# Performance work log

Measured on AMD Instinct MI355X. Metric: run time of the kernel, lower is better.

Reference implementation:

```python
import jax, jax.numpy as jnp
import numpy as np

B, T, D, H = 2, 2048, 1024, 16
DK = D // H


def setup_inputs() -> dict:
    key = jax.random.key(0)
    ks = jax.random.split(key, 9)
    s = 1.0 / np.sqrt(D)
    x = jax.random.normal(ks[0], (B, T, D), dtype=jnp.float32)
    # causal mask (1 = attend, 0 = masked), broadcast over batch and heads
    mask = jnp.tril(jnp.ones((T, T), dtype=jnp.int32))[None, None, :, :]
    Wq = jax.random.uniform(ks[1], (D, D), jnp.float32, -s, s)
    bq = jax.random.uniform(ks[2], (D,), jnp.float32, -s, s)
    Wk = jax.random.uniform(ks[3], (D, D), jnp.float32, -s, s)
    bk = jax.random.uniform(ks[4], (D,), jnp.float32, -s, s)
    Wv = jax.random.uniform(ks[5], (D, D), jnp.float32, -s, s)
    bv = jax.random.uniform(ks[6], (D,), jnp.float32, -s, s)
    Wo = jax.random.uniform(ks[7], (D, D), jnp.float32, -s, s)
    bo = jax.random.uniform(ks[8], (D,), jnp.float32, -s, s)
    return {"x": x, "mask": mask, "Wq": Wq, "bq": bq, "Wk": Wk, "bk": bk,
            "Wv": Wv, "bv": bv, "Wo": Wo, "bo": bo}


def reference(x, mask, Wq, bq, Wk, bk, Wv, bv, Wo, bo):
    # nn.Linear: y = x @ W.T + b
    q = (x @ Wq.T + bq).reshape(B, T, H, DK).transpose(0, 2, 1, 3)  # [B,H,T,DK]
    k = (x @ Wk.T + bk).reshape(B, T, H, DK).transpose(0, 2, 1, 3)
    v = (x @ Wv.T + bv).reshape(B, T, H, DK).transpose(0, 2, 1, 3)
    scores = jnp.einsum('bhqd,bhkd->bhqk', q, k) / np.sqrt(DK).astype(np.float32)
    scores = jnp.where(mask == 0, -jnp.inf, scores)
    attn = jax.nn.softmax(scores, axis=-1)
    out = jnp.einsum('bhqk,bhkd->bhqd', attn, v)  # [B,H,T,DK]
    out = out.transpose(0, 2, 1, 3).reshape(B, T, D)
    return out @ Wo.T + bo
```

## Files before the change

kernel.cpp:

```cpp
#include <hip/hip_runtime.h>

typedef unsigned short u16;
typedef unsigned int u32;
typedef unsigned long long u64;
typedef __attribute__((ext_vector_type(8))) short short8;
typedef __attribute__((ext_vector_type(4))) float f32x4;

#define B_ 2
#define T_ 2048
#define H_ 16
#define DK_ 64
#define QSCALE 0.18033688011112042f

__device__ __forceinline__ u16 f2bf(float f){
  unsigned u = __float_as_uint(f);
  return (u16)((u + 0x7fffu + ((u >> 16) & 1u)) >> 16);
}

__device__ __forceinline__ u32 cvtpk(float lo, float hi){
  u32 r;
  asm("v_cvt_pk_bf16_f32 %0, %1, %2" : "=v"(r) : "v"(lo), "v"(hi));
  return r;
}

#define EXP2(x) __expf(0.6931471805599453f * (x))

__device__ __forceinline__ short8 pack8(const f32x4 a, const f32x4 b){
  union { u32 u[4]; short8 s; } t;
  t.u[0] = cvtpk(a[0], a[1]); t.u[1] = cvtpk(a[2], a[3]);
  t.u[2] = cvtpk(b[0], b[1]); t.u[3] = cvtpk(b[2], b[3]);
  return t.s;
}

#if defined(__has_builtin)
#if __has_builtin(__builtin_amdgcn_global_load_lds)
#define HAS_GLLDS 1
#endif
#endif

#ifdef HAS_GLLDS
__device__ __forceinline__ void gl_lds16(const u16* g, u16* l){
  __builtin_amdgcn_global_load_lds(
      (__attribute__((address_space(1))) void*)(void*)g,
      (__attribute__((address_space(3))) void*)(void*)l, 16, 0, 0);
}
__device__ __forceinline__ void wait_vm4(){ asm volatile("s_waitcnt vmcnt(4)" ::: "memory"); }
__device__ __forceinline__ void wait_vm0(){ asm volatile("s_waitcnt vmcnt(0)" ::: "memory"); }
__device__ __forceinline__ void pipe_bar(){
  asm volatile("" ::: "memory");
  __builtin_amdgcn_s_barrier();
  asm volatile("" ::: "memory");
}
#else
__device__ __forceinline__ void wait_vm4(){}
__device__ __forceinline__ void wait_vm0(){}
__device__ __forceinline__ void pipe_bar(){ __syncthreads(); }
#endif

__global__ __launch_bounds__(256) void conv_all(
    const float* __restrict__ x, const float* __restrict__ wq, const float* __restrict__ wk,
    const float* __restrict__ wv, const float* __restrict__ wo,
    u16* __restrict__ xb, u16* __restrict__ wqb, u16* __restrict__ wkb,
    u16* __restrict__ wvb, u16* __restrict__ wob)
{
  int gid = blockIdx.x * 256 + threadIdx.x;
  const float* src; u16* dst; int off;
  if (gid < 1048576){ src = x; dst = xb; off = gid; }
  else {
    int t = gid - 1048576; int s = t >> 18; off = t & 262143;
    src = (s==0)?wq:((s==1)?wk:((s==2)?wv:wo));
    dst = (s==0)?wqb:((s==1)?wkb:((s==2)?wvb:wob));
  }
  float4 v = ((const float4*)src)[off];
  u64 r = (u64)f2bf(v.x) | ((u64)f2bf(v.y)<<16) | ((u64)f2bf(v.z)<<32) | ((u64)f2bf(v.w)<<48);
  ((u64*)dst)[off] = r;
}

template<int QKV>
__global__ __launch_bounds__(256, 3) void gemm_k5(
    const u16* __restrict__ A,
    const u16* __restrict__ W0, const u16* __restrict__ W1, const u16* __restrict__ W2,
    const float* __restrict__ b0, const float* __restrict__ b1, const float* __restrict__ b2,
    void* __restrict__ o0, void* __restrict__ o1, void* __restrict__ o2)
{
  __shared__ u16 As[3 * 4096];
  __shared__ u16 Bs[3 * 4096];
  const int tid = threadIdx.x;
  const int sel = QKV ? (blockIdx.x >> 3) : 0;
  const int n0 = (blockIdx.x & 7) * 128;
  const int m0 = blockIdx.y * 128;
  const u16* Bw = (sel==0)?W0:((sel==1)?W1:W2);
  const float* bias = (sel==0)?b0:((sel==1)?b1:b2);
  const int w = tid>>6, l = tid&63;
  const int lr = l&15, lg = l>>4;
  const int wm = (w&1)*64, wn = (w>>1)*64;
  const int scol = ((l & 3) ^ ((l >> 3) & 3)) * 8;
  const u16* Ab = A  + (size_t)m0*1024 + (size_t)(l>>2)*1024 + scol;
  const u16* Bb = Bw + (size_t)n0*1024 + (size_t)(l>>2)*1024 + scol;
  const int rsw = (lr >> 1) & 3;
  f32x4 acc[4][4] = {};

  auto STAGE = [&](int t, int pb){
#pragma unroll
    for (int i = 0; i < 2; ++i){
      int c = w*2 + i;
#ifdef HAS_GLLDS
      gl_lds16(Ab + (size_t)(16*c)*1024 + t*32, &As[pb*4096 + c*512]);
      gl_lds16(Bb + (size_t)(16*c)*1024 + t*32, &Bs[pb*4096 + c*512]);
#else
      *(uint4*)&As[pb*4096 + c*512 + l*8] = *(const uint4*)(Ab + (size_t)(16*c)*1024 + t*32);
      *(uint4*)&Bs[pb*4096 + c*512 + l*8] = *(const uint4*)(Bb + (size_t)(16*c)*1024 + t*32);
#endif
    }
  };

  STAGE(0, 0); STAGE(1, 1);
  wait_vm4();
  pipe_bar();
  for (int it = 0; it < 32; ++it){
    const int pb = it % 3;
    if (it < 30) STAGE(it + 2, (it + 2) % 3);
    short8 af[4], bf[4];
#pragma unroll
    for (int mi=0;mi<4;++mi) af[mi] = *(const short8*)&As[pb*4096 + (wm+16*mi+lr)*32 + 8*(lg ^ rsw)];
#pragma unroll
    for (int ni=0;ni<4;++ni) bf[ni] = *(const short8*)&Bs[pb*4096 + (wn+16*ni+lr)*32 + 8*(lg ^ rsw)];
#pragma unroll
    for (int mi=0;mi<4;++mi)
#pragma unroll
      for (int ni=0;ni<4;++ni)
        acc[mi][ni] = __builtin_amdgcn_mfma_f32_16x16x32_bf16(af[mi], bf[ni], acc[mi][ni], 0,0,0);
    if (it < 31){
      if (it < 30) wait_vm4();
      else         wait_vm0();
      pipe_bar();
    }
  }

  float bv[4];
#pragma unroll
  for (int ni=0;ni<4;++ni) bv[ni] = bias[n0+wn+16*ni+lr];
  void* C = QKV ? ((sel==0)?o0:((sel==1)?o1:o2)) : o0;
#pragma unroll
  for (int mi=0;mi<4;++mi)
#pragma unroll
    for (int r=0;r<4;++r){
      const int trow = m0 + wm + 16*mi + 4*lg + r;
#pragma unroll
      for (int ni=0;ni<4;++ni){
        float v = acc[mi][ni][r] + bv[ni];
        int n = n0 + wn + 16*ni + lr;
        if (!QKV){
          ((float*)C)[(size_t)trow*1024 + n] = v;
        } else if (sel == 0){
          ((u16*)C)[(size_t)trow*1024 + n] = f2bf(v * QSCALE);
        } else if (sel == 1){
          int nsw = (n & ~63) | ((n & 63) ^ ((trow & 7) << 3));
          ((u16*)C)[(size_t)trow*1024 + nsw] = f2bf(v);
        } else {
          ((u16*)C)[(size_t)trow*1024 + n] = f2bf(v);
        }
      }
    }
}

__global__ __launch_bounds__(256) void transpose_v128(const u16* __restrict__ V,
                                                      u16* __restrict__ VT){
  __shared__ u16 L[128 * 72];
  const int tid = threadIdx.x;
  const int tc = blockIdx.x, h = blockIdx.y, b = blockIdx.z;
#pragma unroll
  for (int p = 0; p < 4; ++p){
    int row = (tid >> 3) + 32 * p, g = tid & 7;
    *(uint4*)&L[row * 72 + g * 8] =
        *(const uint4*)(V + ((size_t)(b * T_ + tc * 128 + row) * H_ + h) * DK_ + g * 8);
  }
  __syncthreads();
#pragma unroll
  for (int p = 0; p < 4; ++p){
    int d = tid >> 2, g8 = (tid & 3) + 4 * p;
    union { uint4 u; u16 s[8]; } tv;
#pragma unroll
    for (int i = 0; i < 8; ++i){
      int pp = 8 * g8 + i;
      int tl = 32 * (pp >> 5) + 16 * ((pp >> 2) & 1) + 4 * ((pp >> 3) & 3) + (pp & 3);
      tv.s[i] = L[tl * 72 + d];
    }
    *(uint4*)(VT + ((size_t)(b * H_ + h) * DK_ + d) * T_ + tc * 128 + ((8 * g8) ^ ((d & 7) << 3))) = tv.u;
  }
}

__global__ __launch_bounds__(256, 2) void attn_v7(
    const u16* __restrict__ Q, const u16* __restrict__ K,
    const u16* __restrict__ VT, u16* __restrict__ O)
{
  __shared__ u16 Ks[2][128 * 64];
  __shared__ u16 VTs[2][64 * 128];
  const int tid = threadIdx.x;
  const int w = tid >> 6, l = tid & 63;
  const int lr = l & 15, lg = l >> 4;
  const int h = blockIdx.y, b = blockIdx.z;
  const int qtb = (b == 0) ? blockIdx.x : (15 - blockIdx.x);
  const int q0 = qtb * 128;
  const int wrow0 = q0 + 32 * w;
  const size_t kbase = ((size_t)(b * T_) * H_ + h) * DK_;
  const size_t vbase = (size_t)(b * H_ + h) * DK_ * (size_t)T_;

  auto STAGE = [&](int kt, int pb){
#pragma unroll
    for (int p = 0; p < 4; ++p){
      int kr0 = 32 * w + 8 * p;
#ifdef HAS_GLLDS
      gl_lds16(K + kbase + (size_t)(kt * 128 + kr0 + (l >> 3)) * 1024 + (l & 7) * 8,
               &Ks[pb][kr0 * 64]);
#else
      *(uint4*)&Ks[pb][(kr0 + (l >> 3)) * 64 + (l & 7) * 8] =
          *(const uint4*)(K + kbase + (size_t)(kt * 128 + kr0 + (l >> 3)) * 1024 + (l & 7) * 8);
#endif
    }
#pragma unroll
    for (int p = 0; p < 4; ++p){
      int dr0 = 16 * w + 4 * p;
#ifdef HAS_GLLDS
      gl_lds16(VT + vbase + (size_t)(dr0 + (l >> 4)) * T_ + kt * 128 + (l & 15) * 8,
               &VTs[pb][dr0 * 128]);
#else
      *(uint4*)&VTs[pb][(dr0 + (l >> 4)) * 128 + (l & 15) * 8] =
          *(const uint4*)(VT + vbase + (size_t)(dr0 + (l >> 4)) * T_ + kt * 128 + (l & 15) * 8);
#endif
    }
  };

  short8 qf[2][2];
#pragma unroll
  for (int mi = 0; mi < 2; ++mi)
#pragma unroll
    for (int s = 0; s < 2; ++s)
      qf[mi][s] = *(const short8*)(Q + kbase + (size_t)(wrow0 + 16 * mi + lr) * 1024 + s * 32 + 8 * lg);

  f32x4 acc[2][4] = {};
  float lsum[2] = {0.f, 0.f};
  const int ktend = qtb;

  STAGE(0, 0);
  __syncthreads();
  for (int kt = 0; kt <= ktend; ++kt){
    const int pb = kt & 1;
    if (kt < ktend) STAGE(kt + 1, pb ^ 1);
    const bool diag = (kt == ktend);
    short8 pf[2][4];
#pragma unroll
    for (int jh = 0; jh < 2; ++jh){
      short8 kf[4][2];
#pragma unroll
      for (int j = 0; j < 4; ++j)
#pragma unroll
        for (int s = 0; s < 2; ++s)
          kf[j][s] = *(const short8*)&Ks[pb][((4 * jh + j) * 16 + lr) * 64 + (((4 * s + lg) ^ (lr & 7)) << 3)];
#pragma unroll
      for (int mi = 0; mi < 2; ++mi){
        f32x4 pr[4];
        float lacc = 0.f;
        const int lim = 32 * w + 16 * mi + lr;
#pragma unroll
        for (int j = 0; j < 4; ++j){
          const int j0 = 4 * jh + j;
          f32x4 z = {};
          z = __builtin_amdgcn_mfma_f32_16x16x32_bf16(kf[j][0], qf[mi][0], z, 0, 0, 0);
          z = __builtin_amdgcn_mfma_f32_16x16x32_bf16(kf[j][1], qf[mi][1], z, 0, 0, 0);
#pragma unroll
          for (int r = 0; r < 4; ++r){
            float e = EXP2(z[r]);
            if (diag && (16 * j0 + 4 * lg + r > lim)) e = 0.f;
            pr[j][r] = e;
            lacc += e;
          }
        }
        lsum[mi] += lacc;
        pf[mi][2 * jh]     = pack8(pr[0], pr[1]);
        pf[mi][2 * jh + 1] = pack8(pr[2], pr[3]);
      }
    }
#pragma unroll
    for (int ks = 0; ks < 4; ++ks)
#pragma unroll
      for (int d0 = 0; d0 < 4; ++d0){
        short8 vf = *(const short8*)&VTs[pb][(d0 * 16 + lr) * 128 + (((4 * ks + lg) ^ (lr & 7)) << 3)];
        acc[0][d0] = __builtin_amdgcn_mfma_f32_16x16x32_bf16(pf[0][ks], vf, acc[0][d0], 0, 0, 0);
        acc[1][d0] = __builtin_amdgcn_mfma_f32_16x16x32_bf16(pf[1][ks], vf, acc[1][d0], 0, 0, 0);
      }
    __syncthreads();
  }

#pragma unroll
  for (int mi = 0; mi < 2; ++mi){
    float v = lsum[mi];
    v += __shfl_xor(v, 16);
    v += __shfl_xor(v, 32);
    float inv = 1.0f / v;
    float invr[4];
#pragma unroll
    for (int r = 0; r < 4; ++r) invr[r] = __shfl(inv, 4 * lg + r);
#pragma unroll
    for (int d0 = 0; d0 < 4; ++d0)
#pragma unroll
      for (int r = 0; r < 4; ++r){
        float ov = acc[mi][d0][r] * invr[r];
        O[kbase + (size_t)(wrow0 + 16 * mi + 4 * lg + r) * 1024 + d0 * 16 + lr] = f2bf(ov);
      }
  }
}

extern "C" void kernel_launch(void* const* d_in, const int* in_sizes, int n_in,
                              void* d_out, int out_size, void* d_ws, size_t ws_size,
                              hipStream_t stream)
{
  const float* x  = (const float*)d_in[0];
  const float* Wq = (const float*)d_in[2];
  const float* bq = (const float*)d_in[3];
  const float* Wk = (const float*)d_in[4];
  const float* bk = (const float*)d_in[5];
  const float* Wv = (const float*)d_in[6];
  const float* bv = (const float*)d_in[7];
  const float* Wo = (const float*)d_in[8];
  const float* bo = (const float*)d_in[9];

  char* ws = (char*)d_ws;
  u16* xb  = (u16*)(ws + 0);
  u16* wqb = (u16*)(ws + 8388608);
  u16* wkb = (u16*)(ws + 10485760);
  u16* wvb = (u16*)(ws + 12582912);
  u16* wob = (u16*)(ws + 14680064);
  u16* qb  = (u16*)(ws + 16777216);
  u16* kb  = (u16*)(ws + 25165824);
  u16* vb  = (u16*)(ws + 33554432);
  u16* vtb = xb;
  u16* ab  = vb;

  conv_all<<<8192, 256, 0, stream>>>(x, Wq, Wk, Wv, Wo, xb, wqb, wkb, wvb, wob);

  gemm_k5<1><<<dim3(24, 32), 256, 0, stream>>>(
      xb, wqb, wkb, wvb, bq, bk, bv, (void*)qb, (void*)kb, (void*)vb);

  transpose_v128<<<dim3(T_/128, H_, B_), 256, 0, stream>>>(vb, vtb);

  attn_v7<<<dim3(T_/128, H_, B_), 256, 0, stream>>>(qb, kb, vtb, ab);

  gemm_k5<0><<<dim3(8, 32), 256, 0, stream>>>(
      ab, wob, wob, wob, bo, bo, bo, d_out, d_out, d_out);
}
```

Before: 115.5 us.

## Use 256x256-tile 8-wave QKV GEMM with K=64 double buffering

Replaces the 128x128-tile QKV projection GEMM with a 256x256-tile, 512-thread kernel. It uses K-step 64, XOR-swizzled LDS and a double buffer whose next-tile loads are interleaved with MFMA quarters under raised wave priority. The larger tile raises operand reuse and halves the K-loop count. The trade-off is a grid of only 192 blocks on a many-CU device, plus higher LDS and register pressure. The output-projection GEMM is split into its own specialised non-template kernel.

```diff
diff --git a/kernel.cpp b/kernel.cpp
--- a/kernel.cpp
+++ b/kernel.cpp
@@ -76,21 +76,119 @@
   ((u64*)dst)[off] = r;
 }
 
-template<int QKV>
-__global__ __launch_bounds__(256, 3) void gemm_k5(
+__global__ __launch_bounds__(512, 2) void gemm_qkv8(
     const u16* __restrict__ A,
     const u16* __restrict__ W0, const u16* __restrict__ W1, const u16* __restrict__ W2,
     const float* __restrict__ b0, const float* __restrict__ b1, const float* __restrict__ b2,
-    void* __restrict__ o0, void* __restrict__ o1, void* __restrict__ o2)
+    u16* __restrict__ o0, u16* __restrict__ o1, u16* __restrict__ o2)
+{
+  __shared__ u16 As[2][256 * 64];
+  __shared__ u16 Bs[2][256 * 64];
+  const int tid = threadIdx.x;
+  const int w = tid >> 6, l = tid & 63;
+  const int lr = l & 15, lg = l >> 4;
+  const int sel = blockIdx.x >> 2;
+  const int n0 = (blockIdx.x & 3) * 256, m0 = blockIdx.y * 256;
+  const u16* Bw = (sel==0)?W0:((sel==1)?W1:W2);
+  const float* bias = (sel==0)?b0:((sel==1)?b1:b2);
+  u16* C = (sel==0)?o0:((sel==1)?o1:o2);
+  const int wm = (w >> 2) * 128, wn = (w & 3) * 64;
+  const int srow = l >> 3;
+  const int schunk = ((l & 7) ^ (l >> 3)) * 8;
+  const u16* Asrc = A  + (size_t)(m0 + srow) * 1024 + schunk;
+  const u16* Bsrc = Bw + (size_t)(n0 + srow) * 1024 + schunk;
+
+  auto SA = [&](int kt, int c, int pb){
+    const int r0 = 32 * w + 8 * c;
+#ifdef HAS_GLLDS
+    gl_lds16(Asrc + (size_t)r0 * 1024 + kt * 64, &As[pb][r0 * 64]);
+#else
+    *(uint4*)&As[pb][r0 * 64 + l * 8] = *(const uint4*)(Asrc + (size_t)r0 * 1024 + kt * 64);
+#endif
+  };
+  auto SB = [&](int kt, int c, int pb){
+    const int r0 = 32 * w + 8 * c;
+#ifdef HAS_GLLDS
+    gl_lds16(Bsrc + (size_t)r0 * 1024 + kt * 64, &Bs[pb][r0 * 64]);
+#else
+    *(uint4*)&Bs[pb][r0 * 64 + l * 8] = *(const uint4*)(Bsrc + (size_t)r0 * 1024 + kt * 64);
+#endif
+  };
+
+  f32x4 acc[8][4] = {};
+
+#pragma unroll
+  for (int c = 0; c < 4; ++c){ SA(0, c, 0); SB(0, c, 0); }
+  wait_vm0();
+  pipe_bar();
+
+  for (int kt = 0; kt < 16; ++kt){
+    const int pb = kt & 1;
+    short8 bfa[4][2];
+#pragma unroll
+    for (int q = 0; q < 4; ++q){
+      if (q == 0){
+#pragma unroll
+        for (int fn = 0; fn < 4; ++fn)
+#pragma unroll
+          for (int s = 0; s < 2; ++s)
+            bfa[fn][s] = *(const short8*)&Bs[pb][(wn + 16*fn + lr) * 64 + (((4*s + lg) ^ (lr & 7)) << 3)];
+      }
+      short8 af[2][2];
+#pragma unroll
+      for (int mi = 0; mi < 2; ++mi)
+#pragma unroll
+        for (int s = 0; s < 2; ++s)
+          af[mi][s] = *(const short8*)&As[pb][(wm + 16*(2*q + mi) + lr) * 64 + (((4*s + lg) ^ (lr & 7)) << 3)];
+      if (kt < 15){ SA(kt + 1, q, pb ^ 1); SB(kt + 1, q, pb ^ 1); }
+      __builtin_amdgcn_s_barrier();
+      __builtin_amdgcn_s_setprio(1);
+#pragma unroll
+      for (int mi = 0; mi < 2; ++mi)
+#pragma unroll
+        for (int fn = 0; fn < 4; ++fn)
+#pragma unroll
+          for (int s = 0; s < 2; ++s)
+            acc[2*q + mi][fn] = __builtin_amdgcn_mfma_f32_16x16x32_bf16(
+                af[mi][s], bfa[fn][s], acc[2*q + mi][fn], 0, 0, 0);
+      __builtin_amdgcn_s_setprio(0);
+      if (q == 3 && kt < 15) wait_vm0();
+      __builtin_amdgcn_s_barrier();
+    }
+  }
+
+  float bv[4];
+#pragma unroll
+  for (int fn = 0; fn < 4; ++fn) bv[fn] = bias[n0 + wn + 16*fn + lr];
+#pragma unroll
+  for (int fm = 0; fm < 8; ++fm)
+#pragma unroll
+    for (int r = 0; r < 4; ++r){
+      const int trow = m0 + wm + 16*fm + 4*lg + r;
+#pragma unroll
+      for (int fn = 0; fn < 4; ++fn){
+        float v = acc[fm][fn][r] + bv[fn];
+        int n = n0 + wn + 16*fn + lr;
+        if (sel == 0){
+          C[(size_t)trow * 1024 + n] = f2bf(v * QSCALE);
+        } else if (sel == 1){
+          int nsw = (n & ~63) | ((n & 63) ^ ((trow & 7) << 3));
+          C[(size_t)trow * 1024 + nsw] = f2bf(v);
+        } else {
+          C[(size_t)trow * 1024 + n] = f2bf(v);
+        }
+      }
+    }
+}
+
+__global__ __launch_bounds__(256, 3) void gemm_o(
+    const u16* __restrict__ A, const u16* __restrict__ Bw,
+    const float* __restrict__ bias, float* __restrict__ C)
 {
   __shared__ u16 As[3 * 4096];
   __shared__ u16 Bs[3 * 4096];
   const int tid = threadIdx.x;
-  const int sel = QKV ? (blockIdx.x >> 3) : 0;
-  const int n0 = (blockIdx.x & 7) * 128;
-  const int m0 = blockIdx.y * 128;
-  const u16* Bw = (sel==0)?W0:((sel==1)?W1:W2);
-  const float* bias = (sel==0)?b0:((sel==1)?b1:b2);
+  const int n0 = blockIdx.x * 128, m0 = blockIdx.y * 128;
   const int w = tid>>6, l = tid&63;
   const int lr = l&15, lg = l>>4;
   const int wm = (w&1)*64, wn = (w>>1)*64;
@@ -140,27 +238,14 @@
   float bv[4];
 #pragma unroll
   for (int ni=0;ni<4;++ni) bv[ni] = bias[n0+wn+16*ni+lr];
-  void* C = QKV ? ((sel==0)?o0:((sel==1)?o1:o2)) : o0;
 #pragma unroll
   for (int mi=0;mi<4;++mi)
 #pragma unroll
     for (int r=0;r<4;++r){
       const int trow = m0 + wm + 16*mi + 4*lg + r;
 #pragma unroll
-      for (int ni=0;ni<4;++ni){
-        float v = acc[mi][ni][r] + bv[ni];
-        int n = n0 + wn + 16*ni + lr;
-        if (!QKV){
-          ((float*)C)[(size_t)trow*1024 + n] = v;
-        } else if (sel == 0){
-          ((u16*)C)[(size_t)trow*1024 + n] = f2bf(v * QSCALE);
-        } else if (sel == 1){
-          int nsw = (n & ~63) | ((n & 63) ^ ((trow & 7) << 3));
-          ((u16*)C)[(size_t)trow*1024 + nsw] = f2bf(v);
-        } else {
-          ((u16*)C)[(size_t)trow*1024 + n] = f2bf(v);
-        }
-      }
+      for (int ni=0;ni<4;++ni)
+        C[(size_t)trow*1024 + n0 + wn + 16*ni + lr] = acc[mi][ni][r] + bv[ni];
     }
 }
 
@@ -339,13 +424,12 @@
 
   conv_all<<<8192, 256, 0, stream>>>(x, Wq, Wk, Wv, Wo, xb, wqb, wkb, wvb, wob);
 
-  gemm_k5<1><<<dim3(24, 32), 256, 0, stream>>>(
-      xb, wqb, wkb, wvb, bq, bk, bv, (void*)qb, (void*)kb, (void*)vb);
+  gemm_qkv8<<<dim3(12, 16), 512, 0, stream>>>(
+      xb, wqb, wkb, wvb, bq, bk, bv, qb, kb, vb);
 
   transpose_v128<<<dim3(T_/128, H_, B_), 256, 0, stream>>>(vb, vtb);
 
   attn_v7<<<dim3(T_/128, H_, B_), 256, 0, stream>>>(qb, kb, vtb, ab);
 
-  gemm_k5<0><<<dim3(8, 32), 256, 0, stream>>>(
-      ab, wob, wob, wob, bo, bo, bo, d_out, d_out, d_out);
-}
+  gemm_o<<<dim3(8, 32), 256, 0, stream>>>(ab, wob, bo, (float*)d_out);
+}
```

Result: no change. 117.7 us (+1.9%).
